# Optimization experiments

Measured on AMD Instinct MI355X. Metric: run time of the kernel, lower is better.

## Reference

```python
import jax, jax.numpy as jnp
import numpy as np

V = 32000   # vocab_size
B = 32      # batch_size
T = 128     # seq_length
R = 1024    # rnn_size
L = 4       # effective layers: layer_depth**2 due to double MultiRNNCell wrap in source
EPS = 1e-5
FORGET_BIAS = 1.0


def setup_inputs() -> dict:
    key = jax.random.key(0)
    ks = jax.random.split(key, 5)
    return {
        "input_data": jax.random.randint(ks[0], (B, T), 0, V),
        "embedding": jax.random.uniform(ks[1], (V, R), minval=-1.0, maxval=1.0, dtype=jnp.float32),
        "W": jax.random.normal(ks[2], (L, 2 * R, 4 * R), dtype=jnp.float32) * 0.02,
        "bias": jnp.zeros((L, 4 * R), jnp.float32),
        "ln_g": jnp.ones((L, 5, R), jnp.float32),   # LN scale for i, j, f, o, new_c
        "ln_b": jnp.zeros((L, 5, R), jnp.float32),  # LN shift for i, j, f, o, new_c
        "softmax_w": jax.random.normal(ks[3], (V, R), dtype=jnp.float32) * 0.02,
        "softmax_b": jnp.zeros((V,), jnp.float32),
    }


def _ln(x, g, b):
    m = jnp.mean(x, axis=-1, keepdims=True)
    v = jnp.var(x, axis=-1, keepdims=True)
    return (x - m) * jax.lax.rsqrt(v + EPS) * g + b


def _ln_lstm_layer(xs, W, bias, g, bt):
    """LayerNormalizedLSTMCell scanned over time. xs: [T, B, R] -> [T, B, R]."""
    def step(carry, x):
        c, h = carry
        z = jnp.concatenate([x, h], axis=-1) @ W + bias  # [B, 4R]
        i, j, f, o = jnp.split(z, 4, axis=-1)
        i = _ln(i, g[0], bt[0])
        j = _ln(j, g[1], bt[1])
        f = _ln(f, g[2], bt[2])
        o = _ln(o, g[3], bt[3])
        c = c * jax.nn.sigmoid(f + FORGET_BIAS) + jax.nn.sigmoid(i) * jnp.tanh(j)
        h = jnp.tanh(_ln(c, g[4], bt[4])) * jax.nn.sigmoid(o)
        return (c, h), h

    z0 = jnp.zeros(xs.shape[1:], xs.dtype)
    _, ys = jax.lax.scan(step, (z0, z0), xs)
    return ys


def reference(input_data, embedding, W, bias, ln_g, ln_b, softmax_w, softmax_b):
    xs = embedding[input_data]                 # [B, T, R]
    xs = jnp.transpose(xs, (1, 0, 2))          # [T, B, R] time-major for scan
    for l in range(L):
        xs = _ln_lstm_layer(xs, W[l], bias[l], ln_g[l], ln_b[l])
    out = jnp.transpose(xs, (1, 0, 2)).reshape(-1, R)       # [B*T, R]
    logits = out @ softmax_w.T + softmax_b                  # [B*T, V]
    return logits
```

## Files before the change

kernel.cpp:

```cpp
#include <hip/hip_runtime.h>
#include <hip/hip_bf16.h>


typedef __bf16 bf16x8 __attribute__((ext_vector_type(8)));
typedef __bf16 bf16x4 __attribute__((ext_vector_type(4)));
typedef float  f32x4  __attribute__((ext_vector_type(4)));

#define VOCAB 32000
#define BATCH 32
#define SEQ   128
#define RNN   1024
#define NLAY  4
#define GBLK  128
#define AR_STRIDE 16

__device__ __forceinline__ float sigm(float x) { return 1.f / (1.f + __expf(-x)); }

__device__ __forceinline__ unsigned ald(const unsigned* p) {
    return __hip_atomic_load(p, __ATOMIC_RELAXED, __HIP_MEMORY_SCOPE_AGENT);
}
__device__ __forceinline__ void ast(unsigned* p, unsigned v) {
    __hip_atomic_store(p, v, __ATOMIC_RELAXED, __HIP_MEMORY_SCOPE_AGENT);
}
__device__ __forceinline__ unsigned long long ald64(const unsigned long long* p) {
    return __hip_atomic_load(p, __ATOMIC_RELAXED, __HIP_MEMORY_SCOPE_AGENT);
}
__device__ __forceinline__ void ast64(unsigned long long* p, unsigned long long v) {
    __hip_atomic_store(p, v, __ATOMIC_RELAXED, __HIP_MEMORY_SCOPE_AGENT);
}
__device__ __forceinline__ void astf(float* p, float v) {
    __hip_atomic_store(p, v, __ATOMIC_RELAXED, __HIP_MEMORY_SCOPE_AGENT);
}
__device__ __forceinline__ void drain_vm() {
    asm volatile("s_waitcnt vmcnt(0)" ::: "memory");
}

typedef union { unsigned long long u[2]; f32x4 f; }  U128F;
typedef union { unsigned long long u; bf16x4 v; }    U64B;

__global__ __launch_bounds__(256) void k_cvt_w(const float* __restrict__ W,
                                               __bf16* __restrict__ Wt) {
    __shared__ float lds[64][65];
    const int tid = threadIdx.x, tx = tid & 15, ty = tid >> 4;
    const int n0 = blockIdx.x * 64, k0 = blockIdx.y * 64;
    const size_t l = blockIdx.z;
    const float* src = W + (l * 2048 + (size_t)k0) * 4096 + n0;
#pragma unroll
    for (int rr = 0; rr < 4; ++rr) {
        int kr = rr * 16 + ty;
        f32x4 v = *(const f32x4*)(src + (size_t)kr * 4096 + tx * 4);
        lds[kr][tx*4+0] = v[0]; lds[kr][tx*4+1] = v[1];
        lds[kr][tx*4+2] = v[2]; lds[kr][tx*4+3] = v[3];
    }
    __syncthreads();
    __bf16* dhi = Wt + ((l * 2 + 0) * 4096 + (size_t)n0) * 2048 + k0;
    __bf16* dlo = Wt + ((l * 2 + 1) * 4096 + (size_t)n0) * 2048 + k0;
#pragma unroll
    for (int rr = 0; rr < 4; ++rr) {
        int nr = rr * 16 + ty;
        bf16x4 ohi, olo;
#pragma unroll
        for (int j = 0; j < 4; ++j) {
            float x = lds[tx*4+j][nr];
            __bf16 h = (__bf16)x;
            ohi[j] = h;
            olo[j] = (__bf16)(x - (float)h);
        }
        *(bf16x4*)(dhi + (size_t)nr * 2048 + tx * 4) = ohi;
        *(bf16x4*)(dlo + (size_t)nr * 2048 + tx * 4) = olo;
    }
}

__global__ __launch_bounds__(256) void k_cvt(const float* __restrict__ in,
                                             __bf16* __restrict__ out) {
    size_t i = ((size_t)blockIdx.x * 256 + threadIdx.x) * 8;
    f32x4 v0 = *(const f32x4*)(in + i);
    f32x4 v1 = *(const f32x4*)(in + i + 4);
    bf16x8 o;
    o[0]=(__bf16)v0[0]; o[1]=(__bf16)v0[1]; o[2]=(__bf16)v0[2]; o[3]=(__bf16)v0[3];
    o[4]=(__bf16)v1[0]; o[5]=(__bf16)v1[1]; o[6]=(__bf16)v1[2]; o[7]=(__bf16)v1[3];
    *(bf16x8*)(out + i) = o;
}

__global__ __launch_bounds__(256) void k_embed(const int* __restrict__ idx,
                                               const float* __restrict__ emb,
                                               __bf16* __restrict__ xhi,
                                               __bf16* __restrict__ xlo) {
    const int row = blockIdx.x;
    const int t = row >> 5, b = row & 31;
    const int id = idx[b * SEQ + t];
    const int tid = threadIdx.x;
    f32x4 v = *(const f32x4*)(emb + (size_t)id * RNN + tid * 4);
    bf16x4 hi, lo;
#pragma unroll
    for (int j = 0; j < 4; ++j) {
        __bf16 h = (__bf16)v[j];
        hi[j] = h; lo[j] = (__bf16)(v[j] - (float)h);
    }
    *(bf16x4*)(xhi + (size_t)row * RNN + tid * 4) = hi;
    *(bf16x4*)(xlo + (size_t)row * RNN + tid * 4) = lo;
}

__global__ __launch_bounds__(256) void k_xgemm(const __bf16* __restrict__ xhi,
                                               const __bf16* __restrict__ xlo,
                                               const __bf16* __restrict__ Wt,
                                               const float* __restrict__ bias,
                                               float* __restrict__ zx) {
    __shared__ __bf16 Aim[2][4][4][512];
    __shared__ __bf16 Bim[2][4][4][512];
    const int tid = threadIdx.x;
    const int lane = tid & 63, w = tid >> 6;
    const int g = lane >> 4, q = lane & 15;
    const int n0 = blockIdx.x * 64, m0 = blockIdx.y * 64;
    f32x4 acc[4] = {{0,0,0,0},{0,0,0,0},{0,0,0,0},{0,0,0,0}};

    for (int ch = 0; ch < 8; ++ch) {
        __syncthreads();
        for (int i = tid; i < 2048; i += 256) {
            int pl = i >> 10, rem = i & 1023;
            int r = rem >> 4, cc = rem & 15;
            const __bf16* s = (pl ? xlo : xhi) + (size_t)(m0 + r) * RNN + ch * 128 + cc * 8;
            bf16x8 v = *(const bf16x8*)s;
            *(bf16x8*)&Aim[pl][r >> 4][cc >> 2][(((cc & 3) << 4) + (r & 15)) << 3] = v;
        }
        for (int i = tid; i < 2048; i += 256) {
            int pl = i >> 10, rem = i & 1023;
            int r = rem >> 4, cc = rem & 15;
            const __bf16* s = Wt + ((size_t)(pl ? 4096 : 0) + n0 + r) * 2048 + ch * 128 + cc * 8;
            bf16x8 v = *(const bf16x8*)s;
            *(bf16x8*)&Bim[pl][r >> 4][cc >> 2][(((cc & 3) << 4) + (r & 15)) << 3] = v;
        }
        __syncthreads();
#pragma unroll
        for (int kc = 0; kc < 4; ++kc) {
            bf16x8 bhf = *(const bf16x8*)&Bim[0][w][kc][lane << 3];
            bf16x8 blf = *(const bf16x8*)&Bim[1][w][kc][lane << 3];
#pragma unroll
            for (int mt = 0; mt < 4; ++mt) {
                bf16x8 ahf = *(const bf16x8*)&Aim[0][mt][kc][lane << 3];
                bf16x8 alf = *(const bf16x8*)&Aim[1][mt][kc][lane << 3];
                acc[mt] = __builtin_amdgcn_mfma_f32_16x16x32_bf16(ahf, bhf, acc[mt], 0, 0, 0);
                acc[mt] = __builtin_amdgcn_mfma_f32_16x16x32_bf16(alf, bhf, acc[mt], 0, 0, 0);
                acc[mt] = __builtin_amdgcn_mfma_f32_16x16x32_bf16(ahf, blf, acc[mt], 0, 0, 0);
            }
        }
    }
    const int n = n0 + w * 16 + q;
    const float bv = bias[n];
#pragma unroll
    for (int mt = 0; mt < 4; ++mt)
#pragma unroll
        for (int r = 0; r < 4; ++r) {
            int m = m0 + mt * 16 + g * 4 + r;
            zx[(size_t)m * 4096 + n] = acc[mt][r] + bv;
        }
}

__device__ __forceinline__ void bar_all(unsigned* slots, int bk, int tid,
                                        unsigned gen, bool poll) {
    drain_vm();
    __syncthreads();
    if (tid == 0) ast(&slots[bk * AR_STRIDE], gen);
    if (poll && tid < GBLK) {
        while (ald(&slots[tid * AR_STRIDE]) < gen) __builtin_amdgcn_s_sleep(1);
    }
    __syncthreads();
}
__device__ __forceinline__ void bar_gate(unsigned* slots, int bk, bool arrive,
                                         int tid, unsigned gen) {
    drain_vm();
    __syncthreads();
    if (arrive && tid == 0) ast(&slots[bk * AR_STRIDE], gen);
    if (tid < BATCH) {
        while (ald(&slots[tid * AR_STRIDE]) < gen) __builtin_amdgcn_s_sleep(1);
    }
    __syncthreads();
}

__global__ __launch_bounds__(256, 1) void k_rnn(
        const __bf16* __restrict__ Wl,
        float* __restrict__ zx,
        float* __restrict__ z,
        __bf16* __restrict__ xhi, __bf16* __restrict__ xlo,
        const float* __restrict__ g5, const float* __restrict__ b5,
        unsigned* bar, unsigned gen0,
        const __bf16* __restrict__ Wn,
        const float* __restrict__ bias_n)
{
    __shared__ __bf16 wl[2][32768];
    __shared__ f32x4 pred[2][2][64];
    __shared__ float red[4][8];
    unsigned* bar2 = bar + GBLK * AR_STRIDE;

    const int bk = blockIdx.x, tid = threadIdx.x;
    const int lane = tid & 63, w = tid >> 6;
    const int q = lane & 15, g = lane >> 4;
    const int mt = w & 1, kh = w >> 1;
    const int zr0  = (mt << 4) + (g << 2);

    if (bk >= GBLK) {
        const int hk = bk - GBLK;
        const int ncolh = (hk << 5) + q;
        {
            const __bf16* hi_src = Wn + ((size_t)(hk << 5)) * 2048;
            const __bf16* lo_src = Wn + ((size_t)(4096 + (hk << 5))) * 2048;
            for (int i = tid; i < 8192; i += 256) {
                int pl = i >> 12, rem = i & 4095;
                int r = rem >> 7, cc = rem & 127;
                const __bf16* s = (pl ? lo_src : hi_src) + (size_t)r * 2048 + cc * 8;
                bf16x8 v = *(const bf16x8*)s;
                int rnt = r >> 4, rq = r & 15, kc = cc >> 2, rg = cc & 3;
                *(bf16x8*)&wl[pl][((rnt * 32 + kc) << 9) + ((rg * 16 + rq) << 3)] = v;
            }
        }
        float bv0 = 0.f, bv1 = 0.f;
        if (kh == 0) { bv0 = bias_n[ncolh]; bv1 = bias_n[ncolh + 16]; }
        __syncthreads();
        const __bf16* hb0 = &wl[0][0]        + (lane << 3);
        const __bf16* lb0 = &wl[1][0]        + (lane << 3);
        const __bf16* hb1 = &wl[0][32 << 9]  + (lane << 3);
        const __bf16* lb1 = &wl[1][32 << 9]  + (lane << 3);

        for (int t = 0; t < SEQ; ++t) {
            const unsigned gen = gen0 + (unsigned)t + 1u;
            if (tid < BATCH) {
                while (ald(&bar2[tid * AR_STRIDE]) < gen) __builtin_amdgcn_s_sleep(1);
            }
            __syncthreads();
            const __bf16* ah = xhi + ((size_t)t * BATCH + (mt << 4) + q) * RNN;
            const __bf16* al = xlo + ((size_t)t * BATCH + (mt << 4) + q) * RNN;
            f32x4 a00={0,0,0,0}, a01={0,0,0,0}, a02={0,0,0,0};
            f32x4 a10={0,0,0,0}, a11={0,0,0,0}, a12={0,0,0,0};
            const int k0 = kh << 4;
#pragma unroll 4
            for (int kc = k0; kc < k0 + 16; ++kc) {
                bf16x8 ahf = *(const bf16x8*)(ah + (kc << 5) + (g << 3));
                bf16x8 alf = *(const bf16x8*)(al + (kc << 5) + (g << 3));
                bf16x8 b0h = *(const bf16x8*)(hb0 + (kc << 9));
                bf16x8 b0l = *(const bf16x8*)(lb0 + (kc << 9));
                bf16x8 b1h = *(const bf16x8*)(hb1 + (kc << 9));
                bf16x8 b1l = *(const bf16x8*)(lb1 + (kc << 9));
                a00 = __builtin_amdgcn_mfma_f32_16x16x32_bf16(ahf, b0h, a00, 0, 0, 0);
                a01 = __builtin_amdgcn_mfma_f32_16x16x32_bf16(alf, b0h, a01, 0, 0, 0);
                a02 = __builtin_amdgcn_mfma_f32_16x16x32_bf16(ahf, b0l, a02, 0, 0, 0);
                a10 = __builtin_amdgcn_mfma_f32_16x16x32_bf16(ahf, b1h, a10, 0, 0, 0);
                a11 = __builtin_amdgcn_mfma_f32_16x16x32_bf16(alf, b1h, a11, 0, 0, 0);
                a12 = __builtin_amdgcn_mfma_f32_16x16x32_bf16(ahf, b1l, a12, 0, 0, 0);
            }
            f32x4 s0, s1;
#pragma unroll
            for (int j = 0; j < 4; ++j) {
                s0[j] = a00[j] + a01[j] + a02[j];
                s1[j] = a10[j] + a11[j] + a12[j];
            }
            if (kh == 1) { pred[mt][0][lane] = s0; pred[mt][1][lane] = s1; }
            __syncthreads();
            if (kh == 0) {
                f32x4 p0 = pred[mt][0][lane], p1 = pred[mt][1][lane];
#pragma unroll
                for (int r = 0; r < 4; ++r) {
                    zx[((size_t)t * BATCH + zr0 + r) * 4096 + ncolh]      = s0[r] + p0[r] + bv0;
                    zx[((size_t)t * BATCH + zr0 + r) * 4096 + ncolh + 16] = s1[r] + p1[r] + bv1;
                }
            }
            __syncthreads();
        }
        return;
    }

    const int ncol = (bk << 5) + q;

    {
        const __bf16* hi_src = Wl + ((size_t)(bk << 5)) * 2048 + RNN;
        const __bf16* lo_src = Wl + ((size_t)(4096 + (bk << 5))) * 2048 + RNN;
        for (int i = tid; i < 8192; i += 256) {
            int pl = i >> 12, rem = i & 4095;
            int r = rem >> 7, cc = rem & 127;
            const __bf16* s = (pl ? lo_src : hi_src) + (size_t)r * 2048 + cc * 8;
            bf16x8 v = *(const bf16x8*)s;
            int rnt = r >> 4, rq = r & 15, kc = cc >> 2, rg = cc & 3;
            *(bf16x8*)&wl[pl][((rnt * 32 + kc) << 9) + ((rg * 16 + rq) << 3)] = v;
        }
    }

    const bool is_gate = (bk < BATCH);
    f32x4 gi, bi, gj, bj, gf, bfv, go, bo, g4, b4;
    if (is_gate) {
        gi = *(const f32x4*)(g5 + 0*RNN + tid*4); bi = *(const f32x4*)(b5 + 0*RNN + tid*4);
        gj = *(const f32x4*)(g5 + 1*RNN + tid*4); bj = *(const f32x4*)(b5 + 1*RNN + tid*4);
        gf = *(const f32x4*)(g5 + 2*RNN + tid*4); bfv= *(const f32x4*)(b5 + 2*RNN + tid*4);
        go = *(const f32x4*)(g5 + 3*RNN + tid*4); bo = *(const f32x4*)(b5 + 3*RNN + tid*4);
        g4 = *(const f32x4*)(g5 + 4*RNN + tid*4); b4 = *(const f32x4*)(b5 + 4*RNN + tid*4);
    }
    const float inv = 1.f / (float)RNN;
    f32x4 creg = {0.f, 0.f, 0.f, 0.f};
    __syncthreads();

    const __bf16* bh0 = &wl[0][0]        + (lane << 3);
    const __bf16* bl0 = &wl[1][0]        + (lane << 3);
    const __bf16* bh1 = &wl[0][32 << 9]  + (lane << 3);
    const __bf16* bl1 = &wl[1][32 << 9]  + (lane << 3);

    float zv0[4], zv1[4];
    if (kh == 0) {
        const float* zxp = zx + (size_t)zr0 * 4096 + ncol;
#pragma unroll
        for (int r = 0; r < 4; ++r) {
            zv0[r] = zxp[(size_t)r * 4096];
            zv1[r] = zxp[(size_t)r * 4096 + 16];
        }
    }

    for (int t = 0; t < SEQ; ++t) {
        const unsigned gen = gen0 + (unsigned)t + 1u;
        f32x4 a00={0,0,0,0}, a01={0,0,0,0}, a02={0,0,0,0};
        f32x4 a10={0,0,0,0}, a11={0,0,0,0}, a12={0,0,0,0};
        if (t > 0) {
            const __bf16* ah = xhi + ((size_t)(t - 1) * BATCH + (mt << 4) + q) * RNN;
            const __bf16* al = xlo + ((size_t)(t - 1) * BATCH + (mt << 4) + q) * RNN;
            const int k0 = kh << 4;
#pragma unroll 4
            for (int kc = k0; kc < k0 + 16; ++kc) {
                bf16x8 ahf = *(const bf16x8*)(ah + (kc << 5) + (g << 3));
                bf16x8 alf = *(const bf16x8*)(al + (kc << 5) + (g << 3));
                bf16x8 b0h = *(const bf16x8*)(bh0 + (kc << 9));
                bf16x8 b0l = *(const bf16x8*)(bl0 + (kc << 9));
                bf16x8 b1h = *(const bf16x8*)(bh1 + (kc << 9));
                bf16x8 b1l = *(const bf16x8*)(bl1 + (kc << 9));
                a00 = __builtin_amdgcn_mfma_f32_16x16x32_bf16(ahf, b0h, a00, 0, 0, 0);
                a01 = __builtin_amdgcn_mfma_f32_16x16x32_bf16(alf, b0h, a01, 0, 0, 0);
                a02 = __builtin_amdgcn_mfma_f32_16x16x32_bf16(ahf, b0l, a02, 0, 0, 0);
                a10 = __builtin_amdgcn_mfma_f32_16x16x32_bf16(ahf, b1h, a10, 0, 0, 0);
                a11 = __builtin_amdgcn_mfma_f32_16x16x32_bf16(alf, b1h, a11, 0, 0, 0);
                a12 = __builtin_amdgcn_mfma_f32_16x16x32_bf16(ahf, b1l, a12, 0, 0, 0);
            }
        }
        {
            f32x4 s0, s1;
#pragma unroll
            for (int j = 0; j < 4; ++j) {
                s0[j] = a00[j] + a01[j] + a02[j];
                s1[j] = a10[j] + a11[j] + a12[j];
            }
            if (kh == 1) { pred[mt][0][lane] = s0; pred[mt][1][lane] = s1; }
            __syncthreads();
            if (kh == 0) {
                f32x4 p0 = pred[mt][0][lane], p1 = pred[mt][1][lane];
#pragma unroll
                for (int r = 0; r < 4; ++r) {
                    astf(&z[(size_t)(zr0 + r) * 4096 + ncol],      s0[r] + p0[r] + zv0[r]);
                    astf(&z[(size_t)(zr0 + r) * 4096 + ncol + 16], s1[r] + p1[r] + zv1[r]);
                }
            }
        }
        bar_all(bar, bk, tid, gen, is_gate);

        if (kh == 0 && t + 1 < SEQ) {
            const float* zxp = zx + ((size_t)(t + 1) * BATCH + zr0) * 4096 + ncol;
#pragma unroll
            for (int r = 0; r < 4; ++r) {
                zv0[r] = zxp[(size_t)r * 4096];
                zv1[r] = zxp[(size_t)r * 4096 + 16];
            }
        }

        if (is_gate) {
            const int b = bk;
            const float* zrow = z + (size_t)b * 4096 + tid * 4;
            auto ld4 = [&](const float* p) -> f32x4 {
                U128F x;
                x.u[0] = ald64((const unsigned long long*)p);
                x.u[1] = ald64((const unsigned long long*)p + 1);
                return x.f;
            };
            f32x4 zi = ld4(zrow), zjv = ld4(zrow + 1024),
                  zfv = ld4(zrow + 2048), zov = ld4(zrow + 3072);
            float s[8];
            s[0] = zi[0]+zi[1]+zi[2]+zi[3];
            s[1] = zi[0]*zi[0]+zi[1]*zi[1]+zi[2]*zi[2]+zi[3]*zi[3];
            s[2] = zjv[0]+zjv[1]+zjv[2]+zjv[3];
            s[3] = zjv[0]*zjv[0]+zjv[1]*zjv[1]+zjv[2]*zjv[2]+zjv[3]*zjv[3];
            s[4] = zfv[0]+zfv[1]+zfv[2]+zfv[3];
            s[5] = zfv[0]*zfv[0]+zfv[1]*zfv[1]+zfv[2]*zfv[2]+zfv[3]*zfv[3];
            s[6] = zov[0]+zov[1]+zov[2]+zov[3];
            s[7] = zov[0]*zov[0]+zov[1]*zov[1]+zov[2]*zov[2]+zov[3]*zov[3];
#pragma unroll
            for (int o = 32; o; o >>= 1)
#pragma unroll
                for (int i = 0; i < 8; ++i) s[i] += __shfl_xor(s[i], o);
            if (lane == 0) {
#pragma unroll
                for (int i = 0; i < 8; ++i) red[w][i] = s[i];
            }
            __syncthreads();
            float tot[8];
#pragma unroll
            for (int i = 0; i < 8; ++i) tot[i] = red[0][i]+red[1][i]+red[2][i]+red[3][i];

            float mi = tot[0]*inv, ri = rsqrtf(tot[1]*inv - mi*mi + 1e-5f);
            float mj = tot[2]*inv, rj = rsqrtf(tot[3]*inv - mj*mj + 1e-5f);
            float mf = tot[4]*inv, rf = rsqrtf(tot[5]*inv - mf*mf + 1e-5f);
            float mo = tot[6]*inv, ro = rsqrtf(tot[7]*inv - mo*mo + 1e-5f);

            f32x4 onrm;
            float cs = 0.f, cq = 0.f;
#pragma unroll
            for (int j = 0; j < 4; ++j) {
                float iv = (zi[j]-mi)*ri*gi[j] + bi[j];
                float jv = (zjv[j]-mj)*rj*gj[j] + bj[j];
                float fv = (zfv[j]-mf)*rf*gf[j] + bfv[j];
                float ov = (zov[j]-mo)*ro*go[j] + bo[j];
                float cc = creg[j] * sigm(fv + 1.0f) + sigm(iv) * tanhf(jv);
                creg[j] = cc; onrm[j] = ov;
                cs += cc; cq += cc*cc;
            }

            __syncthreads();
            float s2a = cs, s2b = cq;
#pragma unroll
            for (int o = 32; o; o >>= 1) { s2a += __shfl_xor(s2a, o); s2b += __shfl_xor(s2b, o); }
            if (lane == 0) { red[w][0] = s2a; red[w][1] = s2b; }
            __syncthreads();
            float mc = (red[0][0]+red[1][0]+red[2][0]+red[3][0]) * inv;
            float vc = (red[0][1]+red[1][1]+red[2][1]+red[3][1]) * inv - mc*mc;
            float rc = rsqrtf(vc + 1e-5f);

            bf16x4 hh, hl;
#pragma unroll
            for (int j = 0; j < 4; ++j) {
                float cn = (creg[j]-mc)*rc*g4[j] + b4[j];
                float h = tanhf(cn) * sigm(onrm[j]);
                __bf16 a = (__bf16)h;
                hh[j] = a; hl[j] = (__bf16)(h - (float)a);
            }
            U64B ph, pl;
            ph.v = hh; pl.v = hl;
            ast64((unsigned long long*)&xhi[((size_t)t * BATCH + b) * RNN + tid * 4], ph.u);
            ast64((unsigned long long*)&xlo[((size_t)t * BATCH + b) * RNN + tid * 4], pl.u);
        }
        bar_gate(bar2, bk, is_gate, tid, gen);
    }
}

__global__ __launch_bounds__(256) void k_proj(const __bf16* __restrict__ xs,
                                              const __bf16* __restrict__ wv,
                                              const float* __restrict__ sb,
                                              float* __restrict__ out) {
    __shared__ __bf16 Asm[2][8][512];
    __shared__ __bf16 Bsm[2][8][512];
    const int tid = threadIdx.x;
    const int lane = tid & 63, w = tid >> 6;
    const int wm = w & 1, wn = w >> 1;
    const int bid = blockIdx.x;
    const int swz = (bid & 7) * 1000 + (bid >> 3);
    const int m0 = (swz & 31) << 7;
    const int n0 = (swz >> 5) << 7;
    const int mb = m0 >> 7;

    const int lr = lane >> 2, cc4 = lane & 3;
    const __bf16* asrc[2];
    const __bf16* bsrc[2];
#pragma unroll
    for (int p = 0; p < 2; ++p) {
        int st = p * 4 + w;
        asrc[p] = xs + (size_t)((st * 16 + lr) * 32 + mb) * RNN + cc4 * 8;
        bsrc[p] = wv + (size_t)(n0 + st * 16 + lr) * RNN + cc4 * 8;
    }
    const int gidx = cc4 * 16 + lr;

    f32x4 acc[4][4];
#pragma unroll
    for (int i = 0; i < 4; ++i)
#pragma unroll
        for (int j = 0; j < 4; ++j) acc[i][j] = (f32x4){0.f, 0.f, 0.f, 0.f};

    bf16x8 ar[2], br[2];
#pragma unroll
    for (int p = 0; p < 2; ++p) {
        ar[p] = *(const bf16x8*)(asrc[p]);
        br[p] = *(const bf16x8*)(bsrc[p]);
    }
#pragma unroll
    for (int p = 0; p < 2; ++p) {
        int st = p * 4 + w;
        *(bf16x8*)&Asm[0][st][gidx * 8] = ar[p];
        *(bf16x8*)&Bsm[0][st][gidx * 8] = br[p];
    }
    __syncthreads();

    for (int s = 0; s < 32; ++s) {
        const int buf = s & 1;
        if (s + 1 < 32) {
            const int k0 = (s + 1) * 32;
#pragma unroll
            for (int p = 0; p < 2; ++p) {
                ar[p] = *(const bf16x8*)(asrc[p] + k0);
                br[p] = *(const bf16x8*)(bsrc[p] + k0);
            }
        }
        bf16x8 af[4], bfr[4];
#pragma unroll
        for (int i = 0; i < 4; ++i) {
            af[i]  = *(const bf16x8*)&Asm[buf][wm * 4 + i][lane * 8];
            bfr[i] = *(const bf16x8*)&Bsm[buf][wn * 4 + i][lane * 8];
        }
#pragma unroll
        for (int mi = 0; mi < 4; ++mi)
#pragma unroll
            for (int ni = 0; ni < 4; ++ni)
                acc[mi][ni] = __builtin_amdgcn_mfma_f32_16x16x32_bf16(
                    af[mi], bfr[ni], acc[mi][ni], 0, 0, 0);
        if (s + 1 < 32) {
#pragma unroll
            for (int p = 0; p < 2; ++p) {
                int st = p * 4 + w;
                *(bf16x8*)&Asm[buf ^ 1][st][gidx * 8] = ar[p];
                *(bf16x8*)&Bsm[buf ^ 1][st][gidx * 8] = br[p];
            }
        }
        __syncthreads();
    }

    const int q = lane & 15, g = lane >> 4;
#pragma unroll
    for (int ni = 0; ni < 4; ++ni) {
        const int n = n0 + wn * 64 + ni * 16 + q;
        const float bv = sb[n];
#pragma unroll
        for (int mi = 0; mi < 4; ++mi) {
            const int mbase = m0 + wm * 64 + mi * 16 + g * 4;
#pragma unroll
            for (int r = 0; r < 4; ++r)
                __builtin_nontemporal_store(acc[mi][ni][r] + bv,
                                            &out[(size_t)(mbase + r) * VOCAB + n]);
        }
    }
}

extern "C" void kernel_launch(void* const* d_in, const int* in_sizes, int n_in,
                              void* d_out, int out_size, void* d_ws, size_t ws_size,
                              hipStream_t stream) {
    const int*   input = (const int*)  d_in[0];
    const float* emb   = (const float*)d_in[1];
    const float* W     = (const float*)d_in[2];
    const float* bias  = (const float*)d_in[3];
    const float* ln_g  = (const float*)d_in[4];
    const float* ln_b  = (const float*)d_in[5];
    const float* smw   = (const float*)d_in[6];
    const float* smb   = (const float*)d_in[7];
    float* out = (float*)d_out;

    char* p = (char*)d_ws;
    auto alloc = [&](size_t bytes) { char* r = p; p += (bytes + 255) & ~(size_t)255; return r; };
    __bf16* Wt   = (__bf16*)alloc((size_t)NLAY * 2 * 4096 * 2048 * 2);
    __bf16* smwb = (__bf16*)alloc((size_t)VOCAB * RNN * 2);
    __bf16* xhi  = (__bf16*)alloc((size_t)SEQ * BATCH * RNN * 2);
    __bf16* xlo  = (__bf16*)alloc((size_t)SEQ * BATCH * RNN * 2);
    float*  zx   = (float*) alloc((size_t)SEQ * BATCH * 4096 * 4);
    float*  z    = (float*) alloc((size_t)BATCH * 4096 * 4);
    unsigned* bar= (unsigned*)alloc(2 * GBLK * AR_STRIDE * 4);

    hipMemsetAsync(bar, 0, 2 * GBLK * AR_STRIDE * 4, stream);

    k_cvt_w<<<dim3(64, 32, NLAY), 256, 0, stream>>>(W, Wt);
    k_cvt<<<(VOCAB * RNN) / (8 * 256), 256, 0, stream>>>(smw, smwb);
    k_embed<<<SEQ * BATCH, 256, 0, stream>>>(input, emb, xhi, xlo);

    k_xgemm<<<dim3(64, 64), 256, 0, stream>>>(xhi, xlo, Wt, bias, zx);

    for (int l = 0; l < NLAY; ++l) {
        const __bf16* Wl  = Wt + (size_t)l * 2 * 4096 * 2048;
        const float*  gl  = ln_g + (size_t)l * 5 * RNN;
        const float*  bbl = ln_b + (size_t)l * 5 * RNN;
        const int lnext = (l + 1 < NLAY) ? (l + 1) : l;
        const __bf16* Wn  = Wt + (size_t)lnext * 2 * 4096 * 2048;
        const float*  bn  = bias + (size_t)lnext * 4096;
        {
            const __bf16* Wl_ = Wl;
            float* zx_ = zx;
            float* z_ = z;
            __bf16 *xhi_ = xhi, *xlo_ = xlo;
            const float *gl_ = gl, *bbl_ = bbl;
            unsigned* bar_ = bar;
            unsigned gen0 = (unsigned)(l * SEQ);
            const __bf16* Wn_ = Wn;
            const float* bn_ = bn;
            void* args[] = {(void*)&Wl_, (void*)&zx_, (void*)&z_,
                            (void*)&xhi_, (void*)&xlo_, (void*)&gl_, (void*)&bbl_,
                            (void*)&bar_, (void*)&gen0, (void*)&Wn_, (void*)&bn_};
            int nblk = (l + 1 < NLAY) ? 2 * GBLK : GBLK;
            hipLaunchCooperativeKernel((const void*)k_rnn,
                                       dim3(nblk), dim3(256), args, 0, stream);
        }
    }
    k_proj<<<dim3(8000), 256, 0, stream>>>(xhi, smwb, smb, out);
}
```

Before: 6.106 ms.

## Replace global barriers with fine-grained per-producer flag waits in RNN kernel

Replaces the two all-block barriers per timestep with point-to-point dataflow waits. Each thread now polls only the flag of the producer block whose data it needs: the gate row for h, or the column block for each z quarter. GEMM blocks no longer wait for every gate block, and gate blocks no longer wait for every GEMM block, so stages can overlap and a straggler only delays the blocks that depend on it. The cost is more spin-polling from many threads, plus reliance on relaxed atomics and the drain for memory ordering; there is also a possible hazard of producers overwriting buffers before consumers finish reading them.

```diff
diff --git a/kernel.cpp b/kernel.cpp
--- a/kernel.cpp
+++ b/kernel.cpp
@@ -156,25 +156,10 @@
         }
 }
 
-__device__ __forceinline__ void bar_all(unsigned* slots, int bk, int tid,
-                                        unsigned gen, bool poll) {
+__device__ __forceinline__ void arrive(unsigned* slots, int bk, int tid, unsigned gen) {
     drain_vm();
     __syncthreads();
     if (tid == 0) ast(&slots[bk * AR_STRIDE], gen);
-    if (poll && tid < GBLK) {
-        while (ald(&slots[tid * AR_STRIDE]) < gen) __builtin_amdgcn_s_sleep(1);
-    }
-    __syncthreads();
-}
-__device__ __forceinline__ void bar_gate(unsigned* slots, int bk, bool arrive,
-                                         int tid, unsigned gen) {
-    drain_vm();
-    __syncthreads();
-    if (arrive && tid == 0) ast(&slots[bk * AR_STRIDE], gen);
-    if (tid < BATCH) {
-        while (ald(&slots[tid * AR_STRIDE]) < gen) __builtin_amdgcn_s_sleep(1);
-    }
-    __syncthreads();
 }
 
 __global__ __launch_bounds__(256, 1) void k_rnn(
@@ -197,6 +182,7 @@
     const int q = lane & 15, g = lane >> 4;
     const int mt = w & 1, kh = w >> 1;
     const int zr0  = (mt << 4) + (g << 2);
+    const int hrow = (mt << 4) + q;
 
     if (bk >= GBLK) {
         const int hk = bk - GBLK;
@@ -223,12 +209,9 @@
 
         for (int t = 0; t < SEQ; ++t) {
             const unsigned gen = gen0 + (unsigned)t + 1u;
-            if (tid < BATCH) {
-                while (ald(&bar2[tid * AR_STRIDE]) < gen) __builtin_amdgcn_s_sleep(1);
-            }
-            __syncthreads();
-            const __bf16* ah = xhi + ((size_t)t * BATCH + (mt << 4) + q) * RNN;
-            const __bf16* al = xlo + ((size_t)t * BATCH + (mt << 4) + q) * RNN;
+            while (ald(&bar2[hrow * AR_STRIDE]) < gen) __builtin_amdgcn_s_sleep(1);
+            const __bf16* ah = xhi + ((size_t)t * BATCH + hrow) * RNN;
+            const __bf16* al = xlo + ((size_t)t * BATCH + hrow) * RNN;
             f32x4 a00={0,0,0,0}, a01={0,0,0,0}, a02={0,0,0,0};
             f32x4 a10={0,0,0,0}, a11={0,0,0,0}, a12={0,0,0,0};
             const int k0 = kh << 4;
@@ -301,6 +284,8 @@
     const __bf16* bh1 = &wl[0][32 << 9]  + (lane << 3);
     const __bf16* bl1 = &wl[1][32 << 9]  + (lane << 3);
 
+    const int pb = tid >> 3;
+
     float zv0[4], zv1[4];
     if (kh == 0) {
         const float* zxp = zx + (size_t)zr0 * 4096 + ncol;
@@ -316,8 +301,9 @@
         f32x4 a00={0,0,0,0}, a01={0,0,0,0}, a02={0,0,0,0};
         f32x4 a10={0,0,0,0}, a11={0,0,0,0}, a12={0,0,0,0};
         if (t > 0) {
-            const __bf16* ah = xhi + ((size_t)(t - 1) * BATCH + (mt << 4) + q) * RNN;
-            const __bf16* al = xlo + ((size_t)(t - 1) * BATCH + (mt << 4) + q) * RNN;
+            while (ald(&bar2[hrow * AR_STRIDE]) < gen - 1u) __builtin_amdgcn_s_sleep(1);
+            const __bf16* ah = xhi + ((size_t)(t - 1) * BATCH + hrow) * RNN;
+            const __bf16* al = xlo + ((size_t)(t - 1) * BATCH + hrow) * RNN;
             const int k0 = kh << 4;
 #pragma unroll 4
             for (int kc = k0; kc < k0 + 16; ++kc) {
@@ -353,7 +339,7 @@
                 }
             }
         }
-        bar_all(bar, bk, tid, gen, is_gate);
+        arrive(bar, bk, tid, gen);
 
         if (kh == 0 && t + 1 < SEQ) {
             const float* zxp = zx + ((size_t)(t + 1) * BATCH + zr0) * 4096 + ncol;
@@ -373,8 +359,14 @@
                 x.u[1] = ald64((const unsigned long long*)p + 1);
                 return x.f;
             };
-            f32x4 zi = ld4(zrow), zjv = ld4(zrow + 1024),
-                  zfv = ld4(zrow + 2048), zov = ld4(zrow + 3072);
+            while (ald(&bar[(pb      ) * AR_STRIDE]) < gen) __builtin_amdgcn_s_sleep(1);
+            f32x4 zi = ld4(zrow);
+            while (ald(&bar[(pb + 32) * AR_STRIDE]) < gen) __builtin_amdgcn_s_sleep(1);
+            f32x4 zjv = ld4(zrow + 1024);
+            while (ald(&bar[(pb + 64) * AR_STRIDE]) < gen) __builtin_amdgcn_s_sleep(1);
+            f32x4 zfv = ld4(zrow + 2048);
+            while (ald(&bar[(pb + 96) * AR_STRIDE]) < gen) __builtin_amdgcn_s_sleep(1);
+            f32x4 zov = ld4(zrow + 3072);
             float s[8];
             s[0] = zi[0]+zi[1]+zi[2]+zi[3];
             s[1] = zi[0]*zi[0]+zi[1]*zi[1]+zi[2]*zi[2]+zi[3]*zi[3];
@@ -437,8 +429,8 @@
             ph.v = hh; pl.v = hl;
             ast64((unsigned long long*)&xhi[((size_t)t * BATCH + b) * RNN + tid * 4], ph.u);
             ast64((unsigned long long*)&xlo[((size_t)t * BATCH + b) * RNN + tid * 4], pl.u);
-        }
-        bar_gate(bar2, bk, is_gate, tid, gen);
+            arrive(bar2, bk, tid, gen);
+        }
     }
 }
 
```

Result: slower. 6.300 ms (+3.2%).

## Overlap final vocab projection with last LSTM layer via idle cooperative blocks

Applied to the files above, without the earlier changes.

During the last layer's cooperative launch, the second half of the blocks (previously used to precompute the next layer's input GEMM) now compute the softmax projection tiles. Each tile waits on the recurrence barrier generation for its 4-timestep chunk before starting. The separate k_proj launch is removed. This hides projection work behind the serial recurrence. In exchange, only 128 blocks handle 8000 tiles, so the projection tail may extend past the recurrence, and these blocks share CUs with the recurrence blocks.

```diff
diff --git a/kernel.cpp b/kernel.cpp
--- a/kernel.cpp
+++ b/kernel.cpp
@@ -13,6 +13,9 @@
 #define NLAY  4
 #define GBLK  128
 #define AR_STRIDE 16
+#define NTILES_N 250
+#define NTILES_T 32
+#define NTILES  (NTILES_N * NTILES_T)
 
 __device__ __forceinline__ float sigm(float x) { return 1.f / (1.f + __expf(-x)); }
 
@@ -185,7 +188,11 @@
         const float* __restrict__ g5, const float* __restrict__ b5,
         unsigned* bar, unsigned gen0,
         const __bf16* __restrict__ Wn,
-        const float* __restrict__ bias_n)
+        const float* __restrict__ bias_n,
+        int mode,
+        const __bf16* __restrict__ pw,
+        const float* __restrict__ psb,
+        float* __restrict__ pout)
 {
     __shared__ __bf16 wl[2][32768];
     __shared__ f32x4 pred[2][2][64];
@@ -199,6 +206,98 @@
     const int zr0  = (mt << 4) + (g << 2);
 
     if (bk >= GBLK) {
+        if (mode == 1) {
+            __bf16* As = &wl[0][0];
+            __bf16* Bs = &wl[0][16384];
+            const int wm = w & 1, wn = w >> 1;
+            const int lr = lane >> 2, cc4 = lane & 3;
+            const int gidx = cc4 * 16 + lr;
+            for (int tau = bk - GBLK; tau < NTILES; tau += GBLK) {
+                const int tt = tau / NTILES_N;
+                const int n0p = (tau - tt * NTILES_N) * 128;
+                const unsigned gneed = gen0 + 4u * (unsigned)tt + 4u;
+                if (tid < BATCH) {
+                    while (ald(&bar2[tid * AR_STRIDE]) < gneed)
+                        __builtin_amdgcn_s_sleep(1);
+                }
+                __syncthreads();
+                const __bf16* asrc[2];
+                const __bf16* bsrc[2];
+#pragma unroll
+                for (int p2 = 0; p2 < 2; ++p2) {
+                    int st = p2 * 4 + w;
+                    asrc[p2] = xhi + (size_t)(tt * 128 + st * 16 + lr) * RNN + cc4 * 8;
+                    bsrc[p2] = pw  + (size_t)(n0p + st * 16 + lr) * RNN + cc4 * 8;
+                }
+                f32x4 acc[4][4];
+#pragma unroll
+                for (int i = 0; i < 4; ++i)
+#pragma unroll
+                    for (int j = 0; j < 4; ++j) acc[i][j] = (f32x4){0.f,0.f,0.f,0.f};
+                bf16x8 ar[2], br[2];
+#pragma unroll
+                for (int p2 = 0; p2 < 2; ++p2) {
+                    ar[p2] = *(const bf16x8*)(asrc[p2]);
+                    br[p2] = *(const bf16x8*)(bsrc[p2]);
+                }
+#pragma unroll
+                for (int p2 = 0; p2 < 2; ++p2) {
+                    int st = p2 * 4 + w;
+                    *(bf16x8*)&As[st * 512 + gidx * 8] = ar[p2];
+                    *(bf16x8*)&Bs[st * 512 + gidx * 8] = br[p2];
+                }
+                __syncthreads();
+                for (int s = 0; s < 32; ++s) {
+                    const int buf = s & 1;
+                    if (s + 1 < 32) {
+                        const int k0 = (s + 1) * 32;
+#pragma unroll
+                        for (int p2 = 0; p2 < 2; ++p2) {
+                            ar[p2] = *(const bf16x8*)(asrc[p2] + k0);
+                            br[p2] = *(const bf16x8*)(bsrc[p2] + k0);
+                        }
+                    }
+                    bf16x8 af[4], bfr[4];
+#pragma unroll
+                    for (int i = 0; i < 4; ++i) {
+                        af[i]  = *(const bf16x8*)&As[(buf * 8 + wm * 4 + i) * 512 + lane * 8];
+                        bfr[i] = *(const bf16x8*)&Bs[(buf * 8 + wn * 4 + i) * 512 + lane * 8];
+                    }
+#pragma unroll
+                    for (int mi = 0; mi < 4; ++mi)
+#pragma unroll
+                        for (int ni = 0; ni < 4; ++ni)
+                            acc[mi][ni] = __builtin_amdgcn_mfma_f32_16x16x32_bf16(
+                                af[mi], bfr[ni], acc[mi][ni], 0, 0, 0);
+                    if (s + 1 < 32) {
+#pragma unroll
+                        for (int p2 = 0; p2 < 2; ++p2) {
+                            int st = p2 * 4 + w;
+                            *(bf16x8*)&As[((buf ^ 1) * 8 + st) * 512 + gidx * 8] = ar[p2];
+                            *(bf16x8*)&Bs[((buf ^ 1) * 8 + st) * 512 + gidx * 8] = br[p2];
+                        }
+                    }
+                    __syncthreads();
+                }
+#pragma unroll
+                for (int ni = 0; ni < 4; ++ni) {
+                    const int n = n0p + wn * 64 + ni * 16 + q;
+                    const float bv = psb[n];
+#pragma unroll
+                    for (int mi = 0; mi < 4; ++mi) {
+                        const int rb = wm * 64 + mi * 16 + g * 4;
+#pragma unroll
+                        for (int r = 0; r < 4; ++r) {
+                            const int R = tt * 128 + rb + r;
+                            const int m = (R & 31) * 128 + (R >> 5);
+                            __builtin_nontemporal_store(acc[mi][ni][r] + bv,
+                                                        &pout[(size_t)m * VOCAB + n]);
+                        }
+                    }
+                }
+            }
+            return;
+        }
         const int hk = bk - GBLK;
         const int ncolh = (hk << 5) + q;
         {
@@ -442,101 +541,6 @@
     }
 }
 
-__global__ __launch_bounds__(256) void k_proj(const __bf16* __restrict__ xs,
-                                              const __bf16* __restrict__ wv,
-                                              const float* __restrict__ sb,
-                                              float* __restrict__ out) {
-    __shared__ __bf16 Asm[2][8][512];
-    __shared__ __bf16 Bsm[2][8][512];
-    const int tid = threadIdx.x;
-    const int lane = tid & 63, w = tid >> 6;
-    const int wm = w & 1, wn = w >> 1;
-    const int bid = blockIdx.x;
-    const int swz = (bid & 7) * 1000 + (bid >> 3);
-    const int m0 = (swz & 31) << 7;
-    const int n0 = (swz >> 5) << 7;
-    const int mb = m0 >> 7;
-
-    const int lr = lane >> 2, cc4 = lane & 3;
-    const __bf16* asrc[2];
-    const __bf16* bsrc[2];
-#pragma unroll
-    for (int p = 0; p < 2; ++p) {
-        int st = p * 4 + w;
-        asrc[p] = xs + (size_t)((st * 16 + lr) * 32 + mb) * RNN + cc4 * 8;
-        bsrc[p] = wv + (size_t)(n0 + st * 16 + lr) * RNN + cc4 * 8;
-    }
-    const int gidx = cc4 * 16 + lr;
-
-    f32x4 acc[4][4];
-#pragma unroll
-    for (int i = 0; i < 4; ++i)
-#pragma unroll
-        for (int j = 0; j < 4; ++j) acc[i][j] = (f32x4){0.f, 0.f, 0.f, 0.f};
-
-    bf16x8 ar[2], br[2];
-#pragma unroll
-    for (int p = 0; p < 2; ++p) {
-        ar[p] = *(const bf16x8*)(asrc[p]);
-        br[p] = *(const bf16x8*)(bsrc[p]);
-    }
-#pragma unroll
-    for (int p = 0; p < 2; ++p) {
-        int st = p * 4 + w;
-        *(bf16x8*)&Asm[0][st][gidx * 8] = ar[p];
-        *(bf16x8*)&Bsm[0][st][gidx * 8] = br[p];
-    }
-    __syncthreads();
-
-    for (int s = 0; s < 32; ++s) {
-        const int buf = s & 1;
-        if (s + 1 < 32) {
-            const int k0 = (s + 1) * 32;
-#pragma unroll
-            for (int p = 0; p < 2; ++p) {
-                ar[p] = *(const bf16x8*)(asrc[p] + k0);
-                br[p] = *(const bf16x8*)(bsrc[p] + k0);
-            }
-        }
-        bf16x8 af[4], bfr[4];
-#pragma unroll
-        for (int i = 0; i < 4; ++i) {
-            af[i]  = *(const bf16x8*)&Asm[buf][wm * 4 + i][lane * 8];
-            bfr[i] = *(const bf16x8*)&Bsm[buf][wn * 4 + i][lane * 8];
-        }
-#pragma unroll
-        for (int mi = 0; mi < 4; ++mi)
-#pragma unroll
-            for (int ni = 0; ni < 4; ++ni)
-                acc[mi][ni] = __builtin_amdgcn_mfma_f32_16x16x32_bf16(
-                    af[mi], bfr[ni], acc[mi][ni], 0, 0, 0);
-        if (s + 1 < 32) {
-#pragma unroll
-            for (int p = 0; p < 2; ++p) {
-                int st = p * 4 + w;
-                *(bf16x8*)&Asm[buf ^ 1][st][gidx * 8] = ar[p];
-                *(bf16x8*)&Bsm[buf ^ 1][st][gidx * 8] = br[p];
-            }
-        }
-        __syncthreads();
-    }
-
-    const int q = lane & 15, g = lane >> 4;
-#pragma unroll
-    for (int ni = 0; ni < 4; ++ni) {
-        const int n = n0 + wn * 64 + ni * 16 + q;
-        const float bv = sb[n];
-#pragma unroll
-        for (int mi = 0; mi < 4; ++mi) {
-            const int mbase = m0 + wm * 64 + mi * 16 + g * 4;
-#pragma unroll
-            for (int r = 0; r < 4; ++r)
-                __builtin_nontemporal_store(acc[mi][ni][r] + bv,
-                                            &out[(size_t)(mbase + r) * VOCAB + n]);
-        }
-    }
-}
-
 extern "C" void kernel_launch(void* const* d_in, const int* in_sizes, int n_in,
                               void* d_out, int out_size, void* d_ws, size_t ws_size,
                               hipStream_t stream) {
@@ -585,13 +589,16 @@
             unsigned gen0 = (unsigned)(l * SEQ);
             const __bf16* Wn_ = Wn;
             const float* bn_ = bn;
+            int mode = (l + 1 < NLAY) ? 0 : 1;
+            const __bf16* pw_ = smwb;
+            const float* psb_ = smb;
+            float* pout_ = out;
             void* args[] = {(void*)&Wl_, (void*)&zx_, (void*)&z_,
                             (void*)&xhi_, (void*)&xlo_, (void*)&gl_, (void*)&bbl_,
-                            (void*)&bar_, (void*)&gen0, (void*)&Wn_, (void*)&bn_};
-            int nblk = (l + 1 < NLAY) ? 2 * GBLK : GBLK;
+                            (void*)&bar_, (void*)&gen0, (void*)&Wn_, (void*)&bn_,
+                            (void*)&mode, (void*)&pw_, (void*)&psb_, (void*)&pout_};
             hipLaunchCooperativeKernel((const void*)k_rnn,
-                                       dim3(nblk), dim3(256), args, 0, stream);
-        }
-    }
-    k_proj<<<dim3(8000), 256, 0, stream>>>(xhi, smwb, smb, out);
-}
+                                       dim3(2 * GBLK), dim3(256), args, 0, stream);
+        }
+    }
+}
```

Result: faster. 5.746 ms (-5.9%).
